# Kernel tuning notes

Hardware: AMD Instinct MI355X
Metric: run time of the kernel (lower is better)

Reference implementation:

```python
import jax, jax.numpy as jnp
import numpy as np

B, T, D = 4, 2048, 1024
NF = 512
NB = 4
FREQ_SCALE = 0.1


def _w(k, shape, scale):
    return jax.random.normal(k, shape, jnp.float32) * scale


def setup_inputs() -> dict:
    key = jax.random.key(0)
    ks = jax.random.split(key, 16)
    d = D ** -0.5
    inp = {}
    inp['x'] = jax.random.normal(ks[0], (B, T, D), jnp.float32)
    inp['norm_g'] = jnp.ones((D,), jnp.float32)
    inp['norm_b'] = jnp.zeros((D,), jnp.float32)
    inp['Wconcept'] = _w(ks[1], (D, D), d); inp['bconcept'] = jnp.zeros((D,), jnp.float32)
    inp['Wcg'] = _w(ks[2], (D, D), d); inp['bcg'] = jnp.zeros((D,), jnp.float32)
    inp['Wfg'] = _w(ks[3], (NF, D), d); inp['bfg'] = jnp.zeros((NF,), jnp.float32)
    inp['Wtg'] = _w(ks[4], (1, D), d); inp['btg'] = jnp.zeros((1,), jnp.float32)
    inp['Wband'] = _w(ks[5], (NB, D), d); inp['bband'] = jnp.zeros((NB,), jnp.float32)
    inp['Wsp'] = _w(ks[6], (2 * NF, D), d)  # to_spectral, no bias
    inp['freq_importance'] = jnp.ones((NF,), jnp.float32)
    inp['log_decay'] = (jnp.linspace(-3.0, -0.001, NF) + _w(ks[7], (NF,), 0.1)).astype(jnp.float32)
    inp['frequencies'] = ((jnp.arange(NF, dtype=jnp.float32) / NF * 2.0 - 1.0) * 0.2)
    inp['dt'] = jnp.ones((NF,), jnp.float32) * 0.5
    inp['Wgate'] = _w(ks[8], (D, D), d); inp['bgate'] = jnp.zeros((D,), jnp.float32)
    inp['Wfs'] = _w(ks[9], (D, 2 * NF), (2 * NF) ** -0.5)  # from_spectral, no bias
    inp['output_scale'] = jnp.ones((1,), jnp.float32) * 0.5
    inp['norm2_g'] = jnp.ones((D,), jnp.float32)
    inp['norm2_b'] = jnp.zeros((D,), jnp.float32)
    inp['W1'] = _w(ks[10], (4 * D, D), d); inp['b1'] = jnp.zeros((4 * D,), jnp.float32)
    inp['W2'] = _w(ks[11], (D, 4 * D), (4 * D) ** -0.5); inp['b2'] = jnp.zeros((D,), jnp.float32)
    return inp


def _ln(x, g, b):
    m = jnp.mean(x, axis=-1, keepdims=True)
    v = jnp.var(x, axis=-1, keepdims=True)
    return (x - m) * jax.lax.rsqrt(v + 1e-5) * g + b


def reference(x, norm_g, norm_b, Wconcept, bconcept, Wcg, bcg, Wfg, bfg, Wtg, btg,
              Wband, bband, Wsp, freq_importance, log_decay, frequencies, dt,
              Wgate, bgate, Wfs, output_scale, norm2_g, norm2_b, W1, b1, W2, b2):
    b_, t_, _ = x.shape
    nf = log_decay.shape[0]
    nb = Wband.shape[0]
    residual = x
    xn = _ln(x, norm_g, norm_b)

    concept = xn @ Wconcept.T + bconcept
    concept_preserved = concept * jax.nn.sigmoid(xn @ Wcg.T + bcg)

    forget_gates = jax.nn.sigmoid(xn @ Wfg.T + bfg)          # (B,T,NF)
    temporal_strength = jax.nn.sigmoid(xn @ Wtg.T + btg)     # (B,T,1)
    band_strengths = jax.nn.sigmoid(xn @ Wband.T + bband)    # (B,T,NB)

    sp = xn @ Wsp.T                                          # (B,T,2*NF)
    u = jax.lax.complex(sp[..., :nf], sp[..., nf:]) * forget_gates

    decay = jax.nn.sigmoid(log_decay) * (jax.nn.softmax(freq_importance) * nf)
    omega = frequencies * FREQ_SCALE * (jax.nn.sigmoid(dt) * 2.0)
    rot = jax.lax.complex(jnp.cos(omega), jnp.sin(omega))    # (NF,)
    A = decay * rot                                          # (NF,) complex

    band_scale = jnp.repeat(band_strengths, nf // nb, axis=-1)  # (B,T,NF)
    A_exp = A * band_scale                                   # (B,T,NF) complex

    ones_first = jnp.ones((b_, 1, nf), A_exp.dtype)
    powers = jnp.cumprod(jnp.concatenate([ones_first, A_exp[:, :-1, :]], axis=1), axis=1)
    powers = powers * temporal_strength
    kernel = powers * rot

    n_fft = 2 * t_
    Uf = jnp.fft.fft(u, n=n_fft, axis=1)
    Kf = jnp.fft.fft(kernel, n=n_fft, axis=1)
    y = jnp.fft.ifft(Uf * Kf, n=n_fft, axis=1)[:, :t_, :]

    spectral_out = jnp.concatenate([y.real, y.imag], axis=-1)
    y_proj = (spectral_out @ Wfs.T) * output_scale
    gate_values = jax.nn.sigmoid(xn @ Wgate.T + bgate)
    y_gated = (y_proj * gate_values + concept_preserved) / 2.0  # dropout: eval mode

    x2 = residual + y_gated
    xn2 = _ln(x2, norm2_g, norm2_b)
    h = jax.nn.gelu(xn2 @ W1.T + b1, approximate=False)
    return x2 + h @ W2.T + b2
```

## Files before the change

kernel.cpp:

```cpp
#include <hip/hip_runtime.h>
#include <hip/hip_bf16.h>
#include <cstdint>
#include <cstddef>

typedef unsigned short u16;
typedef unsigned int u32;
typedef short bf16x8 __attribute__((ext_vector_type(8)));
typedef float f32x4 __attribute__((ext_vector_type(4)));
typedef float f32x2 __attribute__((ext_vector_type(2)));

static constexpr int Bb = 4, Tt = 2048, Dd = 1024, NFf = 512, NBb = 4;
static constexpr int Mm = Bb * Tt;
static constexpr int NZz = 4736;
static constexpr int Lc = 32;

#define DEV __device__ __forceinline__

typedef const __attribute__((address_space(1))) u32* gas_p;
typedef __attribute__((address_space(3))) u32* las_p;

DEV u16 f2bf(float f) {
    uint32_t u = __float_as_uint(f);
    u = (u + 0x7FFF + ((u >> 16) & 1)) >> 16;
    return (u16)u;
}
DEV float bf2f(u16 h) { return __uint_as_float(((uint32_t)h) << 16); }
DEV float sigm(float x) { return 1.0f / (1.0f + __expf(-x)); }
DEV float gelu_ex(float t) { return 0.5f * t * (1.0f + erff(t * 0.70710678118f)); }

static constexpr int NW0 = NZz * Dd;
static constexpr int NW1 = Dd * 2 * NFf;
static constexpr int NW2 = 4 * Dd * Dd;
static constexpr int NW3 = 4 * Dd * Dd;
static constexpr int NWB_CAT = NW0 / 1024;
static constexpr int NCVT_WFS = NW1 / 1024;
static constexpr int NCVT_MLP = (NW2 + NW3) / 1024;

__global__ __launch_bounds__(256) void prep_all(
    const float* __restrict__ Wconcept, const float* __restrict__ Wcg,
    const float* __restrict__ Wfg, const float* __restrict__ Wgate,
    const float* __restrict__ Wsp, const float* __restrict__ Wtg,
    const float* __restrict__ Wband,
    const float* __restrict__ bconcept, const float* __restrict__ bcg,
    const float* __restrict__ bfg, const float* __restrict__ bgate,
    const float* __restrict__ btg, const float* __restrict__ bband,
    const float* __restrict__ fi, const float* __restrict__ logd,
    const float* __restrict__ freqs, const float* __restrict__ dtv,
    const float* __restrict__ x, const float* __restrict__ norm_g,
    const float* __restrict__ norm_b,
    u16* __restrict__ wcat, float* __restrict__ bias_cat,
    float* __restrict__ rr, float* __restrict__ ri,
    float* __restrict__ Ar, float* __restrict__ Ai,
    u16* __restrict__ xn)
{
    const int bx = blockIdx.x;
    if (bx == 0) {
        __shared__ float red[256];
        int t = threadIdx.x;
        float v0 = fi[t], v1 = fi[t + 256];
        red[t] = fmaxf(v0, v1); __syncthreads();
        for (int s = 128; s; s >>= 1) { if (t < s) red[t] = fmaxf(red[t], red[t + s]); __syncthreads(); }
        float mx = red[0]; __syncthreads();
        float e0 = expf(v0 - mx), e1 = expf(v1 - mx);
        red[t] = e0 + e1; __syncthreads();
        for (int s = 128; s; s >>= 1) { if (t < s) red[t] += red[t + s]; __syncthreads(); }
        float inv = 1.0f / red[0];
#pragma unroll
        for (int k = 0; k < 2; k++) {
            int f = t + k * 256;
            float e = k ? e1 : e0;
            float decay = sigm(logd[f]) * (e * inv * (float)NFf);
            float omega = freqs[f] * 0.1f * (sigm(dtv[f]) * 2.0f);
            float cc = cosf(omega), ss = sinf(omega);
            rr[f] = cc; ri[f] = ss; Ar[f] = decay * cc; Ai[f] = decay * ss;
        }
        return;
    }
    if (bx <= NWB_CAT) {
        const int i = ((bx - 1) * 256 + threadIdx.x) * 4;
        int r = i >> 10, c = i & 1023;
        float4 v = {0.f, 0.f, 0.f, 0.f};
        if      (r < 1024) v = *(const float4*)(Wconcept + r * 1024 + c);
        else if (r < 2048) v = *(const float4*)(Wcg + (r - 1024) * 1024 + c);
        else if (r < 2560) v = *(const float4*)(Wfg + (r - 2048) * 1024 + c);
        else if (r < 3584) v = *(const float4*)(Wgate + (r - 2560) * 1024 + c);
        else if (r < 4608) v = *(const float4*)(Wsp + (r - 3584) * 1024 + c);
        else if (r == 4608) v = *(const float4*)(Wtg + c);
        else if (r < 4613) v = *(const float4*)(Wband + (r - 4609) * 1024 + c);
        *(ushort4*)(wcat + i) = ushort4{f2bf(v.x), f2bf(v.y), f2bf(v.z), f2bf(v.w)};
        if (c == 0) {
            float bv;
            if      (r < 1024) bv = bconcept[r];
            else if (r < 2048) bv = bcg[r - 1024];
            else if (r < 2560) bv = bfg[r - 2048];
            else if (r < 3584) bv = bgate[r - 2560];
            else if (r < 4608) bv = 0.0f;
            else if (r == 4608) bv = btg[0];
            else if (r < 4613) bv = bband[r - 4609];
            else bv = 0.0f;
            bias_cat[r] = bv;
        }
        return;
    }
    const int m = bx - NWB_CAT - 1, tid = threadIdx.x;
    float4 v = ((const float4*)(x + (size_t)m * Dd))[tid];
    float s1 = v.x + v.y + v.z + v.w;
    float s2 = v.x * v.x + v.y * v.y + v.z * v.z + v.w * v.w;
    __shared__ float lds[16];
    for (int o = 32; o; o >>= 1) { s1 += __shfl_down(s1, o); s2 += __shfl_down(s2, o); }
    int lane = tid & 63, w = tid >> 6;
    if (!lane) { lds[w] = s1; lds[8 + w] = s2; }
    __syncthreads();
    s1 = lds[0] + lds[1] + lds[2] + lds[3];
    s2 = lds[8] + lds[9] + lds[10] + lds[11];
    float mean = s1 * (1.0f / Dd);
    float var  = s2 * (1.0f / Dd) - mean * mean;
    float rstd = rsqrtf(var + 1e-5f);
    float4 gv = ((const float4*)norm_g)[tid];
    float4 bv = ((const float4*)norm_b)[tid];
    ushort4 o;
    o.x = f2bf((v.x - mean) * rstd * gv.x + bv.x);
    o.y = f2bf((v.y - mean) * rstd * gv.y + bv.y);
    o.z = f2bf((v.z - mean) * rstd * gv.z + bv.z);
    o.w = f2bf((v.w - mean) * rstd * gv.w + bv.w);
    ((ushort4*)(xn + (size_t)m * Dd))[tid] = o;
}

template<int MODE>
DEV void gemm_body(int m0, int n0,
                   u16* __restrict__ smA, u16* __restrict__ smB,
                   const u16* __restrict__ A, const u16* __restrict__ Bw,
                   const float* __restrict__ bias, const u16* __restrict__ addb,
                   void* __restrict__ Cout, int M, int N, int K,
                   const float* __restrict__ xres = nullptr,
                   const u16* __restrict__ Zf = nullptr,
                   const float* __restrict__ oscp = nullptr,
                   f32x2* __restrict__ psums = nullptr)
{
    const int tid = threadIdx.x;
    const int w = tid >> 6, lane = tid & 63;
    const int wr = w >> 1, wc = w & 1;
    const int quad = lane >> 4, l16 = lane & 15;

    const int r0 = tid >> 3;
    const int cs = (tid & 7) ^ (r0 & 7);
    const u16* gA = A + (size_t)(m0 + r0) * K + cs * 8;
    const u16* gB = Bw + (size_t)(n0 + r0) * K + cs * 8;

    const int swzf = l16 & 7;

    f32x4 acc[4][4];
#pragma unroll
    for (int i = 0; i < 4; i++)
#pragma unroll
        for (int j = 0; j < 4; j++) acc[i][j] = {0.f, 0.f, 0.f, 0.f};

    for (int k0 = 0; k0 < K; k0 += 64) {
        __syncthreads();
#pragma unroll
        for (int j = 0; j < 4; j++) {
            __builtin_amdgcn_global_load_lds((gas_p)(gA + k0 + (size_t)(j * 32) * K),
                                             (las_p)(smA + j * 2048 + tid * 8), 16, 0, 0);
            __builtin_amdgcn_global_load_lds((gas_p)(gB + k0 + (size_t)(j * 32) * K),
                                             (las_p)(smB + j * 2048 + tid * 8), 16, 0, 0);
        }
        __syncthreads();
#pragma unroll
        for (int seg = 0; seg < 2; seg++) {
            bf16x8 af[4], bfv[4];
#pragma unroll
            for (int mi = 0; mi < 4; mi++)
                af[mi] = *(const bf16x8*)&smA[(wr * 64 + mi * 16 + l16) * 64 +
                                              (((seg * 4 + quad) ^ swzf) * 8)];
#pragma unroll
            for (int ni = 0; ni < 4; ni++)
                bfv[ni] = *(const bf16x8*)&smB[(wc * 64 + ni * 16 + l16) * 64 +
                                               (((seg * 4 + quad) ^ swzf) * 8)];
#pragma unroll
            for (int mi = 0; mi < 4; mi++)
#pragma unroll
                for (int ni = 0; ni < 4; ni++)
                    acc[mi][ni] = __builtin_amdgcn_mfma_f32_16x16x32_bf16(
                        af[mi], bfv[ni], acc[mi][ni], 0, 0, 0);
        }
    }

    if constexpr (MODE == 5) {
        const float os = oscp[0];
        float rs1[4][4], rs2[4][4];
#pragma unroll
        for (int mi = 0; mi < 4; mi++)
#pragma unroll
            for (int r = 0; r < 4; r++) { rs1[mi][r] = 0.f; rs2[mi][r] = 0.f; }
#pragma unroll
        for (int mi = 0; mi < 4; mi++) {
#pragma unroll
            for (int r = 0; r < 4; r++) {
                const int gm = m0 + wr * 64 + mi * 16 + quad * 4 + r;
                const u16* zr = Zf + (size_t)gm * NZz;
                const float* xr = xres + (size_t)gm * Dd;
                u16* o = (u16*)Cout;
#pragma unroll
                for (int ni = 0; ni < 4; ni++) {
                    const int gn = n0 + wc * 64 + ni * 16 + l16;
                    float p = acc[mi][ni][r];
                    float concept = bf2f(zr[gn]);
                    float cg   = sigm(bf2f(zr[1024 + gn]));
                    float gate = sigm(bf2f(zr[2560 + gn]));
                    float v = xr[gn] + 0.5f * (p * os * gate + concept * cg);
                    rs1[mi][r] += v; rs2[mi][r] += v * v;
                    o[(size_t)gm * Dd + gn] = f2bf(v);
                }
            }
        }
        const int nch = (n0 + wc * 64) >> 6;
#pragma unroll
        for (int mi = 0; mi < 4; mi++)
#pragma unroll
            for (int r = 0; r < 4; r++) {
                float a = rs1[mi][r], b = rs2[mi][r];
#pragma unroll
                for (int o = 1; o < 16; o <<= 1) {
                    a += __shfl_xor(a, o); b += __shfl_xor(b, o);
                }
                if (l16 == 0) {
                    const int gm = m0 + wr * 64 + mi * 16 + quad * 4 + r;
                    psums[(size_t)nch * Mm + gm] = f32x2{a, b};
                }
            }
        return;
    }

#pragma unroll
    for (int mi = 0; mi < 4; mi++) {
#pragma unroll
        for (int ni = 0; ni < 4; ni++) {
            const int gn = n0 + wc * 64 + ni * 16 + l16;
            const int gm0 = m0 + wr * 64 + mi * 16 + quad * 4;
            if constexpr (MODE == 0 || MODE == 2 || MODE == 4) {
                float bv = (MODE == 4) ? 0.0f : bias[gn];
                float t0 = acc[mi][ni][0] + bv, t1 = acc[mi][ni][1] + bv;
                float t2 = acc[mi][ni][2] + bv, t3 = acc[mi][ni][3] + bv;
                if constexpr (MODE == 2) {
                    t0 = gelu_ex(t0); t1 = gelu_ex(t1); t2 = gelu_ex(t2); t3 = gelu_ex(t3);
                }
                __hip_bfloat162 h01 = __float22bfloat162_rn(float2{t0, t1});
                __hip_bfloat162 h23 = __float22bfloat162_rn(float2{t2, t3});
                __hip_bfloat16* o = (__hip_bfloat16*)Cout;
                o[(size_t)(gm0 + 0) * N + gn] = h01.x;
                o[(size_t)(gm0 + 1) * N + gn] = h01.y;
                o[(size_t)(gm0 + 2) * N + gn] = h23.x;
                o[(size_t)(gm0 + 3) * N + gn] = h23.y;
            } else {
#pragma unroll
                for (int r = 0; r < 4; r++) {
                    const int gm = gm0 + r;
                    ((float*)Cout)[(size_t)gm * N + gn] =
                        acc[mi][ni][r] + bias[gn] + bf2f(addb[(size_t)gm * N + gn]);
                }
            }
        }
    }
}

template<int MODE>
__global__ __launch_bounds__(256, 3) void gemm_bt(
    const u16* __restrict__ A, const u16* __restrict__ Bw,
    const float* __restrict__ bias, const u16* __restrict__ addb,
    void* __restrict__ Cout, int M, int N, int K)
{
    __shared__ __align__(16) u16 smA[128 * 64];
    __shared__ __align__(16) u16 smB[128 * 64];
    gemm_body<MODE>(blockIdx.x * 128, blockIdx.y * 128, smA, smB,
                    A, Bw, bias, addb, Cout, M, N, K);
}

static constexpr int NG2 = (Mm / 128) * (NZz / 128);
__global__ __launch_bounds__(256, 3) void gemm_cvt0(
    const u16* __restrict__ A, const u16* __restrict__ Bw,
    const float* __restrict__ bias, void* __restrict__ Cout,
    int M, int N, int K,
    const float* __restrict__ Wfs, u16* __restrict__ wfs)
{
    const int bid = blockIdx.x;
    if (bid < NG2) {
        __shared__ __align__(16) u16 smA[128 * 64];
        __shared__ __align__(16) u16 smB[128 * 64];
        gemm_body<0>((bid & 63) * 128, (bid >> 6) * 128, smA, smB,
                     A, Bw, bias, nullptr, Cout, M, N, K);
        return;
    }
    const int i = (bid - NG2) * 1024 + threadIdx.x * 4;
    float4 v = *(const float4*)(Wfs + i);
    *(ushort4*)(wfs + i) = ushort4{f2bf(v.x), f2bf(v.y), f2bf(v.z), f2bf(v.w)};
}

static constexpr int NG5 = (Mm / 128) * (Dd / 128);
__global__ __launch_bounds__(256, 3) void gemm_cvt5(
    const u16* __restrict__ A, const u16* __restrict__ Bw,
    void* __restrict__ Cout, int M, int N, int K,
    const float* __restrict__ xres, const u16* __restrict__ Zf,
    const float* __restrict__ oscp, f32x2* __restrict__ psums,
    const float* __restrict__ W1, const float* __restrict__ W2,
    u16* __restrict__ w1b, u16* __restrict__ w2b)
{
    const int bid = blockIdx.x;
    if (bid < NG5) {
        __shared__ __align__(16) u16 smA[128 * 64];
        __shared__ __align__(16) u16 smB[128 * 64];
        gemm_body<5>((bid & 63) * 128, (bid >> 6) * 128, smA, smB,
                     A, Bw, nullptr, nullptr, Cout, M, N, K,
                     xres, Zf, oscp, psums);
        return;
    }
    const int i = (bid - NG5) * 1024 + threadIdx.x * 4;
    if (i < NW2) {
        float4 v = *(const float4*)(W1 + i);
        *(ushort4*)(w1b + i) = ushort4{f2bf(v.x), f2bf(v.y), f2bf(v.z), f2bf(v.w)};
    } else {
        int j = i - NW2;
        float4 v = *(const float4*)(W2 + j);
        *(ushort4*)(w2b + j) = ushort4{f2bf(v.x), f2bf(v.y), f2bf(v.z), f2bf(v.w)};
    }
}

__global__ __launch_bounds__(256) void ln2_finish(
    const f32x2* __restrict__ psums, const u16* __restrict__ x2b,
    const float* __restrict__ g2, const float* __restrict__ b2v,
    u16* __restrict__ xn2)
{
    const int m = blockIdx.x, tid = threadIdx.x;
    __shared__ float sm[2];
    if (tid < 64) {
        f32x2 p = (tid < 16) ? psums[(size_t)tid * Mm + m] : f32x2{0.f, 0.f};
        for (int o = 8; o; o >>= 1) { p.x += __shfl_down(p.x, o); p.y += __shfl_down(p.y, o); }
        if (tid == 0) { sm[0] = p.x; sm[1] = p.y; }
    }
    __syncthreads();
    float mean = sm[0] * (1.0f / Dd);
    float var  = sm[1] * (1.0f / Dd) - mean * mean;
    float rstd = rsqrtf(var + 1e-5f);
    ushort4 h = ((const ushort4*)(x2b + (size_t)m * Dd))[tid];
    float4 gv = ((const float4*)g2)[tid];
    float4 bv = ((const float4*)b2v)[tid];
    ushort4 o;
    o.x = f2bf((bf2f(h.x) - mean) * rstd * gv.x + bv.x);
    o.y = f2bf((bf2f(h.y) - mean) * rstd * gv.y + bv.y);
    o.z = f2bf((bf2f(h.z) - mean) * rstd * gv.z + bv.z);
    o.w = f2bf((bf2f(h.w) - mean) * rstd * gv.w + bv.w);
    ((ushort4*)(xn2 + (size_t)m * Dd))[tid] = o;
}

__global__ __launch_bounds__(256) void conv_kernel(
    const u16* __restrict__ Z,
    const float* __restrict__ Ar, const float* __restrict__ Ai,
    const float* __restrict__ rr, const float* __restrict__ ri,
    u16* __restrict__ spec)
{
    __shared__ ushort2 su[96 * 64];
    __shared__ float stsv[Lc], sbsv[Lc];
    const int tid = threadIdx.x;
    const int fl = tid & 63;
    const int ty = tid >> 6;
    const int f0 = blockIdx.x * 64;
    const int t0 = blockIdx.y * 64;
    const int b  = blockIdx.z;
    const int band = f0 >> 7;

    if (tid < Lc) {
        stsv[tid] = sigm(bf2f(Z[(size_t)(b * Tt + tid) * NZz + 4608]));
    } else if (tid < 2 * Lc) {
        int tau = tid - Lc;
        sbsv[tau] = sigm(bf2f(Z[(size_t)(b * Tt + tau) * NZz + 4609 + band]));
    }
    for (int i = tid; i < 96 * 32; i += 256) {
        int r = i >> 5, fp = (i & 31) * 2;
        int t = t0 - 32 + r;
        ushort4 v{0, 0, 0, 0};
        if (t >= 0) {
            const u16* zr = Z + (size_t)(b * Tt + t) * NZz;
            ushort2 fg2 = *(const ushort2*)(zr + 2048 + f0 + fp);
            ushort2 sr2 = *(const ushort2*)(zr + 3584 + f0 + fp);
            ushort2 si2 = *(const ushort2*)(zr + 4096 + f0 + fp);
            float g0 = sigm(bf2f(fg2.x)), g1 = sigm(bf2f(fg2.y));
            v.x = f2bf(bf2f(sr2.x) * g0); v.y = f2bf(bf2f(si2.x) * g0);
            v.z = f2bf(bf2f(sr2.y) * g1); v.w = f2bf(bf2f(si2.y) * g1);
        }
        *(ushort4*)&su[r * 64 + fp] = v;
    }
    __syncthreads();

    const float ar = Ar[f0 + fl], ai = Ai[f0 + fl];
    const float cr = rr[f0 + fl], ci = ri[f0 + fl];
    float Pr = 1.0f, Pi = 0.0f;

    const int tl0 = 32 + ty * 16;
    f32x2 win[16], y[16];
#pragma unroll
    for (int j = 0; j < 16; j++) {
        ushort2 h = su[(tl0 + j) * 64 + fl];
        win[j] = f32x2{bf2f(h.x), bf2f(h.y)};
        y[j] = f32x2{0.f, 0.f};
    }
#pragma unroll
    for (int tau = 0; tau < Lc; tau++) {
        float tsv = stsv[tau];
        float kr = tsv * (cr * Pr - ci * Pi);
        float ki = tsv * (cr * Pi + ci * Pr);
#pragma unroll
        for (int j = 0; j < 16; j++) {
            y[j].x += win[j].x * kr - win[j].y * ki;
            y[j].y += win[j].x * ki + win[j].y * kr;
        }
#pragma unroll
        for (int j = 15; j >= 1; j--) win[j] = win[j - 1];
        ushort2 h = su[(tl0 - tau - 1) * 64 + fl];
        win[0] = f32x2{bf2f(h.x), bf2f(h.y)};
        float bsv = sbsv[tau];
        float er = ar * bsv, ei = ai * bsv;
        float nPr = Pr * er - Pi * ei;
        float nPi = Pr * ei + Pi * er;
        Pr = nPr; Pi = nPi;
    }
#pragma unroll
    for (int j = 0; j < 16; j++) {
        size_t row = (size_t)(b * Tt + t0 + ty * 16 + j);
        spec[row * (2 * NFf) + f0 + fl]       = f2bf(y[j].x);
        spec[row * (2 * NFf) + NFf + f0 + fl] = f2bf(y[j].y);
    }
}

extern "C" void kernel_launch(void* const* d_in, const int* in_sizes, int n_in,
                              void* d_out, int out_size, void* d_ws, size_t ws_size,
                              hipStream_t stream)
{
    const float* x        = (const float*)d_in[0];
    const float* norm_g   = (const float*)d_in[1];
    const float* norm_b   = (const float*)d_in[2];
    const float* Wconcept = (const float*)d_in[3];
    const float* bconcept = (const float*)d_in[4];
    const float* Wcg      = (const float*)d_in[5];
    const float* bcg      = (const float*)d_in[6];
    const float* Wfg      = (const float*)d_in[7];
    const float* bfg      = (const float*)d_in[8];
    const float* Wtg      = (const float*)d_in[9];
    const float* btg      = (const float*)d_in[10];
    const float* Wband    = (const float*)d_in[11];
    const float* bband    = (const float*)d_in[12];
    const float* Wsp      = (const float*)d_in[13];
    const float* fi       = (const float*)d_in[14];
    const float* logd     = (const float*)d_in[15];
    const float* freqs    = (const float*)d_in[16];
    const float* dtv      = (const float*)d_in[17];
    const float* Wgate    = (const float*)d_in[18];
    const float* bgate    = (const float*)d_in[19];
    const float* Wfs      = (const float*)d_in[20];
    const float* osc      = (const float*)d_in[21];
    const float* n2g      = (const float*)d_in[22];
    const float* n2b      = (const float*)d_in[23];
    const float* W1       = (const float*)d_in[24];
    const float* b1       = (const float*)d_in[25];
    const float* W2       = (const float*)d_in[26];
    const float* b2       = (const float*)d_in[27];

    char* ws = (char*)d_ws;
    size_t off = 0;
    auto alloc = [&](size_t bytes) { size_t c = off; off += (bytes + 255) & ~(size_t)255; return c; };
    size_t o_wcat = alloc((size_t)NZz * Dd * 2);
    size_t o_bias = alloc((size_t)NZz * 4);
    size_t o_wfs  = alloc((size_t)Dd * 2 * NFf * 2);
    size_t o_w1   = alloc((size_t)4 * Dd * Dd * 2);
    size_t o_w2   = alloc((size_t)4 * Dd * Dd * 2);
    size_t o_xn   = alloc((size_t)Mm * Dd * 2);
    size_t o_Z    = alloc((size_t)Mm * NZz * 2);
    size_t o_u    = alloc((size_t)Mm * NFf * 4);
    size_t o_spec = alloc((size_t)Mm * Dd * 2);
    size_t o_ps   = alloc((size_t)16 * Mm * 8);
    size_t o_rr   = alloc(NFf * 4);
    size_t o_ri   = alloc(NFf * 4);
    size_t o_Ar   = alloc(NFf * 4);
    size_t o_Ai   = alloc(NFf * 4);
    if (ws_size < off) return;

    u16*    wcat = (u16*)(ws + o_wcat);
    float*  bias = (float*)(ws + o_bias);
    u16*    wfs  = (u16*)(ws + o_wfs);
    u16*    w1b  = (u16*)(ws + o_w1);
    u16*    w2b  = (u16*)(ws + o_w2);
    u16*    xn   = (u16*)(ws + o_xn);
    u16*    Zb   = (u16*)(ws + o_Z);
    u16*    hb   = (u16*)(ws + o_Z);
    u16*    x2b  = (u16*)(ws + o_u);
    u16*    spec = (u16*)(ws + o_spec);
    u16*    xn2  = (u16*)(ws + o_spec);
    f32x2*  psums = (f32x2*)(ws + o_ps);
    float*  rr   = (float*)(ws + o_rr);
    float*  ri   = (float*)(ws + o_ri);
    float*  Ar   = (float*)(ws + o_Ar);
    float*  Ai   = (float*)(ws + o_Ai);

    prep_all<<<1 + NWB_CAT + Mm, 256, 0, stream>>>(
        Wconcept, Wcg, Wfg, Wgate, Wsp, Wtg, Wband,
        bconcept, bcg, bfg, bgate, btg, bband,
        fi, logd, freqs, dtv,
        x, norm_g, norm_b,
        wcat, bias, rr, ri, Ar, Ai, xn);

    gemm_cvt0<<<NG2 + NCVT_WFS, 256, 0, stream>>>(
        xn, wcat, bias, (void*)Zb, Mm, NZz, Dd, Wfs, wfs);

    conv_kernel<<<dim3(NFf / 64, Tt / 64, Bb), 256, 0, stream>>>(
        Zb, Ar, Ai, rr, ri, spec);

    gemm_cvt5<<<NG5 + NCVT_MLP, 256, 0, stream>>>(
        spec, wfs, (void*)x2b, Mm, Dd, 2 * NFf,
        x, Zb, osc, psums, W1, W2, w1b, w2b);

    ln2_finish<<<Mm, 256, 0, stream>>>(psums, x2b, n2g, n2b, xn2);

    gemm_bt<2><<<dim3(Mm / 128, (4 * Dd) / 128), 256, 0, stream>>>(
        xn2, w1b, b1, nullptr, (void*)hb, Mm, 4 * Dd, Dd);
    gemm_bt<3><<<dim3(Mm / 128, Dd / 128), 256, 0, stream>>>(
        hb, w2b, b2, x2b, d_out, Mm, Dd, 4 * Dd);
}
```

Before: 538.5 us.

## Stage MODE5 epilogue through LDS for coalesced loads; move MLP weight conversion earlier

The fused from-spectral GEMM epilogue now writes its accumulator tile to shared memory as bf16 and re-reads it row-major. Each thread can then issue vectorized, coalesced loads of the residual and Z gate/concept columns and vectorized stores, instead of scattered 2-byte accesses. Per-row LN partial sums are reduced over 128-column chunks, which halves the psums buffer. The W1/W2 bf16 conversion blocks move from the MODE5 launch into the first GEMM launch, so the MODE5 kernel is a plain 2D grid. Costs: extra LDS traffic and syncs, and the GEMM result is rounded to bf16 before the epilogue math.

```diff
diff --git a/kernel.cpp b/kernel.cpp
--- a/kernel.cpp
+++ b/kernel.cpp
@@ -33,8 +33,7 @@
 static constexpr int NW2 = 4 * Dd * Dd;
 static constexpr int NW3 = 4 * Dd * Dd;
 static constexpr int NWB_CAT = NW0 / 1024;
-static constexpr int NCVT_WFS = NW1 / 1024;
-static constexpr int NCVT_MLP = (NW2 + NW3) / 1024;
+static constexpr int NCVT = (NW1 + NW2 + NW3) / 1024;
 
 __global__ __launch_bounds__(256) void prep_all(
     const float* __restrict__ Wconcept, const float* __restrict__ Wcg,
@@ -186,48 +185,64 @@
     }
 
     if constexpr (MODE == 5) {
+        u16* smC = smA;
+        __syncthreads();
+#pragma unroll
+        for (int mi = 0; mi < 4; mi++)
+#pragma unroll
+            for (int ni = 0; ni < 4; ni++) {
+                const int lr = wr * 64 + mi * 16 + quad * 4;
+                const int lc = wc * 64 + ni * 16 + l16;
+#pragma unroll
+                for (int r = 0; r < 4; r++)
+                    smC[(lr + r) * 128 + lc] = f2bf(acc[mi][ni][r]);
+            }
+        __syncthreads();
         const float os = oscp[0];
-        float rs1[4][4], rs2[4][4];
-#pragma unroll
-        for (int mi = 0; mi < 4; mi++)
-#pragma unroll
-            for (int r = 0; r < 4; r++) { rs1[mi][r] = 0.f; rs2[mi][r] = 0.f; }
-#pragma unroll
-        for (int mi = 0; mi < 4; mi++) {
-#pragma unroll
-            for (int r = 0; r < 4; r++) {
-                const int gm = m0 + wr * 64 + mi * 16 + quad * 4 + r;
-                const u16* zr = Zf + (size_t)gm * NZz;
-                const float* xr = xres + (size_t)gm * Dd;
-                u16* o = (u16*)Cout;
-#pragma unroll
-                for (int ni = 0; ni < 4; ni++) {
-                    const int gn = n0 + wc * 64 + ni * 16 + l16;
-                    float p = acc[mi][ni][r];
-                    float concept = bf2f(zr[gn]);
-                    float cg   = sigm(bf2f(zr[1024 + gn]));
-                    float gate = sigm(bf2f(zr[2560 + gn]));
-                    float v = xr[gn] + 0.5f * (p * os * gate + concept * cg);
-                    rs1[mi][r] += v; rs2[mi][r] += v * v;
-                    o[(size_t)gm * Dd + gn] = f2bf(v);
-                }
+        const int tr = tid >> 4, tc = tid & 15;
+        u16* ob = (u16*)Cout;
+#pragma unroll
+        for (int rb = 0; rb < 8; rb++) {
+            const int row = rb * 16 + tr;
+            const int gm = m0 + row;
+            const int gn0 = n0 + tc * 8;
+            const u16* zr = Zf + (size_t)gm * NZz;
+            const float* xr = xres + (size_t)gm * Dd;
+            float4 xv0 = *(const float4*)(xr + gn0);
+            float4 xv1 = *(const float4*)(xr + gn0 + 4);
+            ushort4 c0 = *(const ushort4*)(zr + gn0);
+            ushort4 c1 = *(const ushort4*)(zr + gn0 + 4);
+            ushort4 g0 = *(const ushort4*)(zr + 1024 + gn0);
+            ushort4 g1 = *(const ushort4*)(zr + 1024 + gn0 + 4);
+            ushort4 a0 = *(const ushort4*)(zr + 2560 + gn0);
+            ushort4 a1 = *(const ushort4*)(zr + 2560 + gn0 + 4);
+            const u16* pp = &smC[row * 128 + tc * 8];
+            float s1 = 0.f, s2 = 0.f;
+            ushort4 o0, o1;
+#pragma unroll
+            for (int j = 0; j < 4; j++) {
+                float p = bf2f(pp[j]);
+                float v = (&xv0.x)[j] + 0.5f * (p * os * sigm(bf2f((&a0.x)[j])) +
+                                                bf2f((&c0.x)[j]) * sigm(bf2f((&g0.x)[j])));
+                s1 += v; s2 += v * v;
+                (&o0.x)[j] = f2bf(v);
             }
-        }
-        const int nch = (n0 + wc * 64) >> 6;
-#pragma unroll
-        for (int mi = 0; mi < 4; mi++)
-#pragma unroll
-            for (int r = 0; r < 4; r++) {
-                float a = rs1[mi][r], b = rs2[mi][r];
-#pragma unroll
-                for (int o = 1; o < 16; o <<= 1) {
-                    a += __shfl_xor(a, o); b += __shfl_xor(b, o);
-                }
-                if (l16 == 0) {
-                    const int gm = m0 + wr * 64 + mi * 16 + quad * 4 + r;
-                    psums[(size_t)nch * Mm + gm] = f32x2{a, b};
-                }
+#pragma unroll
+            for (int j = 0; j < 4; j++) {
+                float p = bf2f(pp[4 + j]);
+                float v = (&xv1.x)[j] + 0.5f * (p * os * sigm(bf2f((&a1.x)[j])) +
+                                                bf2f((&c1.x)[j]) * sigm(bf2f((&g1.x)[j])));
+                s1 += v; s2 += v * v;
+                (&o1.x)[j] = f2bf(v);
             }
+            *(ushort4*)(ob + (size_t)gm * Dd + gn0)     = o0;
+            *(ushort4*)(ob + (size_t)gm * Dd + gn0 + 4) = o1;
+#pragma unroll
+            for (int o = 1; o < 16; o <<= 1) {
+                s1 += __shfl_xor(s1, o); s2 += __shfl_xor(s2, o);
+            }
+            if (tc == 0) psums[(size_t)(n0 >> 7) * Mm + gm] = f32x2{s1, s2};
+        }
         return;
     }
 
@@ -280,7 +295,9 @@
     const u16* __restrict__ A, const u16* __restrict__ Bw,
     const float* __restrict__ bias, void* __restrict__ Cout,
     int M, int N, int K,
-    const float* __restrict__ Wfs, u16* __restrict__ wfs)
+    const float* __restrict__ Wfs, const float* __restrict__ W1,
+    const float* __restrict__ W2,
+    u16* __restrict__ wfs, u16* __restrict__ w1b, u16* __restrict__ w2b)
 {
     const int bid = blockIdx.x;
     if (bid < NG2) {
@@ -291,37 +308,30 @@
         return;
     }
     const int i = (bid - NG2) * 1024 + threadIdx.x * 4;
-    float4 v = *(const float4*)(Wfs + i);
-    *(ushort4*)(wfs + i) = ushort4{f2bf(v.x), f2bf(v.y), f2bf(v.z), f2bf(v.w)};
-}
-
-static constexpr int NG5 = (Mm / 128) * (Dd / 128);
-__global__ __launch_bounds__(256, 3) void gemm_cvt5(
+    if (i < NW1) {
+        float4 v = *(const float4*)(Wfs + i);
+        *(ushort4*)(wfs + i) = ushort4{f2bf(v.x), f2bf(v.y), f2bf(v.z), f2bf(v.w)};
+    } else if (i < NW1 + NW2) {
+        int j = i - NW1;
+        float4 v = *(const float4*)(W1 + j);
+        *(ushort4*)(w1b + j) = ushort4{f2bf(v.x), f2bf(v.y), f2bf(v.z), f2bf(v.w)};
+    } else {
+        int j = i - NW1 - NW2;
+        float4 v = *(const float4*)(W2 + j);
+        *(ushort4*)(w2b + j) = ushort4{f2bf(v.x), f2bf(v.y), f2bf(v.z), f2bf(v.w)};
+    }
+}
+
+__global__ __launch_bounds__(256, 3) void gemm5_fuse(
     const u16* __restrict__ A, const u16* __restrict__ Bw,
     void* __restrict__ Cout, int M, int N, int K,
     const float* __restrict__ xres, const u16* __restrict__ Zf,
-    const float* __restrict__ oscp, f32x2* __restrict__ psums,
-    const float* __restrict__ W1, const float* __restrict__ W2,
-    u16* __restrict__ w1b, u16* __restrict__ w2b)
-{
-    const int bid = blockIdx.x;
-    if (bid < NG5) {
-        __shared__ __align__(16) u16 smA[128 * 64];
-        __shared__ __align__(16) u16 smB[128 * 64];
-        gemm_body<5>((bid & 63) * 128, (bid >> 6) * 128, smA, smB,
-                     A, Bw, nullptr, nullptr, Cout, M, N, K,
-                     xres, Zf, oscp, psums);
-        return;
-    }
-    const int i = (bid - NG5) * 1024 + threadIdx.x * 4;
-    if (i < NW2) {
-        float4 v = *(const float4*)(W1 + i);
-        *(ushort4*)(w1b + i) = ushort4{f2bf(v.x), f2bf(v.y), f2bf(v.z), f2bf(v.w)};
-    } else {
-        int j = i - NW2;
-        float4 v = *(const float4*)(W2 + j);
-        *(ushort4*)(w2b + j) = ushort4{f2bf(v.x), f2bf(v.y), f2bf(v.z), f2bf(v.w)};
-    }
+    const float* __restrict__ oscp, f32x2* __restrict__ psums)
+{
+    __shared__ __align__(16) u16 smX[128 * 128];
+    gemm_body<5>(blockIdx.x * 128, blockIdx.y * 128, smX, smX + 128 * 64,
+                 A, Bw, nullptr, nullptr, Cout, M, N, K,
+                 xres, Zf, oscp, psums);
 }
 
 __global__ __launch_bounds__(256) void ln2_finish(
@@ -332,8 +342,8 @@
     const int m = blockIdx.x, tid = threadIdx.x;
     __shared__ float sm[2];
     if (tid < 64) {
-        f32x2 p = (tid < 16) ? psums[(size_t)tid * Mm + m] : f32x2{0.f, 0.f};
-        for (int o = 8; o; o >>= 1) { p.x += __shfl_down(p.x, o); p.y += __shfl_down(p.y, o); }
+        f32x2 p = (tid < 8) ? psums[(size_t)tid * Mm + m] : f32x2{0.f, 0.f};
+        for (int o = 4; o; o >>= 1) { p.x += __shfl_down(p.x, o); p.y += __shfl_down(p.y, o); }
         if (tid == 0) { sm[0] = p.x; sm[1] = p.y; }
     }
     __syncthreads();
@@ -475,7 +485,7 @@
     size_t o_Z    = alloc((size_t)Mm * NZz * 2);
     size_t o_u    = alloc((size_t)Mm * NFf * 4);
     size_t o_spec = alloc((size_t)Mm * Dd * 2);
-    size_t o_ps   = alloc((size_t)16 * Mm * 8);
+    size_t o_ps   = alloc((size_t)8 * Mm * 8);
     size_t o_rr   = alloc(NFf * 4);
     size_t o_ri   = alloc(NFf * 4);
     size_t o_Ar   = alloc(NFf * 4);
@@ -506,15 +516,16 @@
         x, norm_g, norm_b,
         wcat, bias, rr, ri, Ar, Ai, xn);
 
-    gemm_cvt0<<<NG2 + NCVT_WFS, 256, 0, stream>>>(
-        xn, wcat, bias, (void*)Zb, Mm, NZz, Dd, Wfs, wfs);
+    gemm_cvt0<<<NG2 + NCVT, 256, 0, stream>>>(
+        xn, wcat, bias, (void*)Zb, Mm, NZz, Dd,
+        Wfs, W1, W2, wfs, w1b, w2b);
 
     conv_kernel<<<dim3(NFf / 64, Tt / 64, Bb), 256, 0, stream>>>(
         Zb, Ar, Ai, rr, ri, spec);
 
-    gemm_cvt5<<<NG5 + NCVT_MLP, 256, 0, stream>>>(
+    gemm5_fuse<<<dim3(Mm / 128, Dd / 128), 256, 0, stream>>>(
         spec, wfs, (void*)x2b, Mm, Dd, 2 * NFf,
-        x, Zb, osc, psums, W1, W2, w1b, w2b);
+        x, Zb, osc, psums);
 
     ln2_finish<<<Mm, 256, 0, stream>>>(psums, x2b, n2g, n2b, xn2);
 
```

New measurement: 497.8 us, median of 2. -7.6%, faster.
